# Kernel tuning notes

Hardware: AMD Instinct MI355X
Metric: run time of the kernel (lower is better)

Reference implementation:

```python
import jax, jax.numpy as jnp
import numpy as np

N_NODES = 10000
N_EDGES = 640000
EMB_DIM = 128
NUM_RELS = 500


def setup_inputs() -> dict:
    key = jax.random.key(0)
    k_h, k_s, k_d, k_e, k_f, k_r = jax.random.split(key, 6)
    h = jax.random.normal(k_h, (N_NODES, EMB_DIM), dtype=jnp.float32)
    src = jax.random.randint(k_s, (N_EDGES,), 0, N_NODES, dtype=jnp.int64)
    dst = jax.random.randint(k_d, (N_EDGES,), 0, N_NODES, dtype=jnp.int64)
    etype = jax.random.randint(k_e, (N_EDGES,), 0, NUM_RELS, dtype=jnp.int64)
    fwd_rel = jax.random.normal(k_f, (NUM_RELS, EMB_DIM), dtype=jnp.float32)
    rev_rel = jax.random.normal(k_r, (NUM_RELS, EMB_DIM), dtype=jnp.float32)
    return {"h": h, "src": src, "dst": dst, "etype": etype,
            "fwd_rel": fwd_rel, "rev_rel": rev_rel}


def reference(h, src, dst, etype, fwd_rel, rev_rel):
    # DistMult forward-direction scoring (num_rels > 1 branch):
    #   w  = fwd_rel[etype]                  -> [E, D]
    #   ht = h[src] * w                      (u_mul_e)
    #   score[e] = <ht[e], h[dst[e]]>        (e_dot_v)
    w = fwd_rel[etype]                       # [E, D] gather
    h_u = h[src]                             # [E, D] gather
    h_v = h[dst]                             # [E, D] gather
    score = jnp.einsum("ed,ed,ed->e", h_u, w, h_v)  # [E]
    return score
```

## Files before the change

### kernel.cpp

```cpp
#include <hip/hip_runtime.h>


constexpr int EMB_DIM  = 128;
constexpr int HALF_DIM = 64;

__global__ __launch_bounds__(256) void distmult_half_kernel(
    const float* __restrict__ h,
    const int*   __restrict__ src,
    const int*   __restrict__ dst,
    const int*   __restrict__ etype,
    const float* __restrict__ fwd_rel,
    float*       __restrict__ partial,
    int n_edges)
{
    const int b    = blockIdx.x;
    const int g    = b >> 3;
    const int r    = b & 7;
    const int half = (r >= 4);
    const int idx  = g * 4 + (r & 3);

    const int team = threadIdx.x >> 4;
    const int lane = threadIdx.x & 15;

    const int e0 = idx * 32 + team * 2;
    const int e1 = e0 + 1;
    if (e0 >= n_edges) return;

    const int doff = half * HALF_DIM + lane * 4;

    const int s0 = src[e0];
    const int d0 = dst[e0];
    const int t0 = etype[e0];

    float4 a0, b0, c0;
    a0 = *reinterpret_cast<const float4*>(h       + (size_t)s0 * EMB_DIM + doff);
    b0 = *reinterpret_cast<const float4*>(fwd_rel + (size_t)t0 * EMB_DIM + doff);
    c0 = *reinterpret_cast<const float4*>(h       + (size_t)d0 * EMB_DIM + doff);

    float acc0 = a0.x * b0.x * c0.x + a0.y * b0.y * c0.y
               + a0.z * b0.z * c0.z + a0.w * b0.w * c0.w;

    float acc1 = 0.0f;
    const bool has1 = (e1 < n_edges);
    if (has1) {
        const int s1 = src[e1];
        const int d1 = dst[e1];
        const int t1 = etype[e1];
        float4 a1 = *reinterpret_cast<const float4*>(h       + (size_t)s1 * EMB_DIM + doff);
        float4 b1 = *reinterpret_cast<const float4*>(fwd_rel + (size_t)t1 * EMB_DIM + doff);
        float4 c1 = *reinterpret_cast<const float4*>(h       + (size_t)d1 * EMB_DIM + doff);
        acc1 = a1.x * b1.x * c1.x + a1.y * b1.y * c1.y
             + a1.z * b1.z * c1.z + a1.w * b1.w * c1.w;
    }

    #pragma unroll
    for (int off = 8; off > 0; off >>= 1) {
        acc0 += __shfl_down(acc0, off, 16);
        acc1 += __shfl_down(acc1, off, 16);
    }

    if (lane == 0) {
        float* p = partial + (size_t)half * n_edges;
        p[e0] = acc0;
        if (has1) p[e1] = acc1;
    }
}

__global__ __launch_bounds__(256) void combine_kernel(
    const float* __restrict__ p, float* __restrict__ out, int n_edges)
{
    const int n4 = n_edges >> 2;
    const float4* p0 = reinterpret_cast<const float4*>(p);
    const float4* p1 = reinterpret_cast<const float4*>(p + n_edges);
    float4* o = reinterpret_cast<float4*>(out);
    for (int i = blockIdx.x * blockDim.x + threadIdx.x; i < n4;
         i += gridDim.x * blockDim.x) {
        float4 x = p0[i], y = p1[i];
        o[i] = make_float4(x.x + y.x, x.y + y.y, x.z + y.z, x.w + y.w);
    }
    for (int i = (n4 << 2) + blockIdx.x * blockDim.x + threadIdx.x; i < n_edges;
         i += gridDim.x * blockDim.x) {
        out[i] = p[i] + p[n_edges + i];
    }
}

__global__ __launch_bounds__(256) void distmult_score_kernel(
    const float* __restrict__ h,
    const int*   __restrict__ src,
    const int*   __restrict__ dst,
    const int*   __restrict__ etype,
    const float* __restrict__ fwd_rel,
    float*       __restrict__ out,
    int n_edges)
{
    const int tid  = blockIdx.x * blockDim.x + threadIdx.x;
    const int lane = threadIdx.x & 63;
    const int half = lane >> 5;
    const int sub  = lane & 31;
    const int edge = (tid >> 6) * 2 + half;
    if (edge >= n_edges) return;

    const int s = src[edge];
    const int d = dst[edge];
    const int e = etype[edge];

    const float4 a = reinterpret_cast<const float4*>(h       + (size_t)s * EMB_DIM)[sub];
    const float4 b = reinterpret_cast<const float4*>(fwd_rel + (size_t)e * EMB_DIM)[sub];
    const float4 c = reinterpret_cast<const float4*>(h       + (size_t)d * EMB_DIM)[sub];

    float acc = a.x * b.x * c.x + a.y * b.y * c.y
              + a.z * b.z * c.z + a.w * b.w * c.w;
    #pragma unroll
    for (int off = 16; off > 0; off >>= 1)
        acc += __shfl_down(acc, off, 32);
    if (sub == 0) out[edge] = acc;
}

extern "C" void kernel_launch(void* const* d_in, const int* in_sizes, int n_in,
                              void* d_out, int out_size, void* d_ws, size_t ws_size,
                              hipStream_t stream) {
    const float* h       = (const float*)d_in[0];
    const int*   src     = (const int*)d_in[1];
    const int*   dst     = (const int*)d_in[2];
    const int*   etype   = (const int*)d_in[3];
    const float* fwd_rel = (const float*)d_in[4];
    float* out = (float*)d_out;

    const int n_edges = in_sizes[1];
    const size_t need = (size_t)2 * n_edges * sizeof(float);

    if (ws_size >= need) {
        float* partial = (float*)d_ws;
        const int blocks_per_half = (n_edges + 31) / 32;
        const int groups = (blocks_per_half + 3) / 4;
        const int grid = groups * 8;
        distmult_half_kernel<<<grid, 256, 0, stream>>>(
            h, src, dst, etype, fwd_rel, partial, n_edges);
        const int cgrid = ((n_edges / 4) + 255) / 256;
        combine_kernel<<<cgrid, 256, 0, stream>>>(partial, out, n_edges);
    } else {
        const int grid = (n_edges + 7) / 8;
        distmult_score_kernel<<<grid, 256, 0, stream>>>(
            h, src, dst, etype, fwd_rel, out, n_edges);
    }
}
```

Measured before the change: 111.9 us.

## Stage relation table half in LDS and use a persistent grid with 4 edges per team

The half-dimension scoring kernel becomes persistent: 256 blocks of 1024 threads. Each block first copies its half of the relation embedding table into shared memory (about 128KB), so relation-vector lookups read LDS instead of global memory. Each 16-lane team then loops over groups of 4 edges, loading indices with int4 vector loads, issuing 8 row gathers at once and writing the 4 scores with one float4 store. The risks are the per-block startup cost of filling LDS before any work begins, lower occupancy from one large LDS-heavy block per CU, and a fallback path now needed when the relation count exceeds 500.

```diff
diff --git a/kernel.cpp b/kernel.cpp
--- a/kernel.cpp
+++ b/kernel.cpp
@@ -1,68 +1,101 @@
 #include <hip/hip_runtime.h>
 
 
-constexpr int EMB_DIM  = 128;
-constexpr int HALF_DIM = 64;
+constexpr int EMB_DIM      = 128;
+constexpr int HALF_DIM     = 64;
+constexpr int MAX_RELS     = 500;
+constexpr int BLOCKS_TOTAL = 256;
+constexpr int BLK_THREADS  = 1024;
 
-__global__ __launch_bounds__(256) void distmult_half_kernel(
+__global__ __launch_bounds__(BLK_THREADS) void distmult_lds_kernel(
     const float* __restrict__ h,
     const int*   __restrict__ src,
     const int*   __restrict__ dst,
     const int*   __restrict__ etype,
     const float* __restrict__ fwd_rel,
     float*       __restrict__ partial,
-    int n_edges)
+    int n_edges, int n_rels)
 {
+    __shared__ float w_lds[MAX_RELS * HALF_DIM];
+
     const int b    = blockIdx.x;
     const int g    = b >> 3;
     const int r    = b & 7;
     const int half = (r >= 4);
     const int idx  = g * 4 + (r & 3);
 
+    {
+        const int slots = n_rels * (HALF_DIM / 4);
+        for (int s = threadIdx.x; s < slots; s += BLK_THREADS) {
+            const int row = s >> 4;
+            const int c   = s & 15;
+            float4 v = *reinterpret_cast<const float4*>(
+                fwd_rel + (size_t)row * EMB_DIM + half * HALF_DIM + c * 4);
+            *reinterpret_cast<float4*>(w_lds + row * HALF_DIM + c * 4) = v;
+        }
+    }
+    __syncthreads();
+
     const int team = threadIdx.x >> 4;
     const int lane = threadIdx.x & 15;
 
-    const int e0 = idx * 32 + team * 2;
-    const int e1 = e0 + 1;
-    if (e0 >= n_edges) return;
+    const float* hp = h + half * HALF_DIM + lane * 4;
+    const float* wl = w_lds + lane * 4;
+    float* p = partial + (size_t)half * n_edges;
 
-    const int doff = half * HALF_DIM + lane * 4;
+    const int stride = (BLOCKS_TOTAL / 2) * (BLK_THREADS / 16) * 4;
 
-    const int s0 = src[e0];
-    const int d0 = dst[e0];
-    const int t0 = etype[e0];
+    for (int e0 = idx * (BLK_THREADS / 16) * 4 + team * 4; e0 < n_edges;
+         e0 += stride) {
+        if (e0 + 3 < n_edges) {
+            const int4 s4 = *reinterpret_cast<const int4*>(src   + e0);
+            const int4 d4 = *reinterpret_cast<const int4*>(dst   + e0);
+            const int4 t4 = *reinterpret_cast<const int4*>(etype + e0);
 
-    float4 a0, b0, c0;
-    a0 = *reinterpret_cast<const float4*>(h       + (size_t)s0 * EMB_DIM + doff);
-    b0 = *reinterpret_cast<const float4*>(fwd_rel + (size_t)t0 * EMB_DIM + doff);
-    c0 = *reinterpret_cast<const float4*>(h       + (size_t)d0 * EMB_DIM + doff);
+            float4 a0 = *reinterpret_cast<const float4*>(hp + (size_t)s4.x * EMB_DIM);
+            float4 a1 = *reinterpret_cast<const float4*>(hp + (size_t)s4.y * EMB_DIM);
+            float4 a2 = *reinterpret_cast<const float4*>(hp + (size_t)s4.z * EMB_DIM);
+            float4 a3 = *reinterpret_cast<const float4*>(hp + (size_t)s4.w * EMB_DIM);
+            float4 c0 = *reinterpret_cast<const float4*>(hp + (size_t)d4.x * EMB_DIM);
+            float4 c1 = *reinterpret_cast<const float4*>(hp + (size_t)d4.y * EMB_DIM);
+            float4 c2 = *reinterpret_cast<const float4*>(hp + (size_t)d4.z * EMB_DIM);
+            float4 c3 = *reinterpret_cast<const float4*>(hp + (size_t)d4.w * EMB_DIM);
 
-    float acc0 = a0.x * b0.x * c0.x + a0.y * b0.y * c0.y
-               + a0.z * b0.z * c0.z + a0.w * b0.w * c0.w;
+            float4 b0 = *reinterpret_cast<const float4*>(wl + (size_t)t4.x * HALF_DIM);
+            float4 b1 = *reinterpret_cast<const float4*>(wl + (size_t)t4.y * HALF_DIM);
+            float4 b2 = *reinterpret_cast<const float4*>(wl + (size_t)t4.z * HALF_DIM);
+            float4 b3 = *reinterpret_cast<const float4*>(wl + (size_t)t4.w * HALF_DIM);
 
-    float acc1 = 0.0f;
-    const bool has1 = (e1 < n_edges);
-    if (has1) {
-        const int s1 = src[e1];
-        const int d1 = dst[e1];
-        const int t1 = etype[e1];
-        float4 a1 = *reinterpret_cast<const float4*>(h       + (size_t)s1 * EMB_DIM + doff);
-        float4 b1 = *reinterpret_cast<const float4*>(fwd_rel + (size_t)t1 * EMB_DIM + doff);
-        float4 c1 = *reinterpret_cast<const float4*>(h       + (size_t)d1 * EMB_DIM + doff);
-        acc1 = a1.x * b1.x * c1.x + a1.y * b1.y * c1.y
-             + a1.z * b1.z * c1.z + a1.w * b1.w * c1.w;
-    }
+            float acc0 = a0.x*b0.x*c0.x + a0.y*b0.y*c0.y + a0.z*b0.z*c0.z + a0.w*b0.w*c0.w;
+            float acc1 = a1.x*b1.x*c1.x + a1.y*b1.y*c1.y + a1.z*b1.z*c1.z + a1.w*b1.w*c1.w;
+            float acc2 = a2.x*b2.x*c2.x + a2.y*b2.y*c2.y + a2.z*b2.z*c2.z + a2.w*b2.w*c2.w;
+            float acc3 = a3.x*b3.x*c3.x + a3.y*b3.y*c3.y + a3.z*b3.z*c3.z + a3.w*b3.w*c3.w;
 
-    #pragma unroll
-    for (int off = 8; off > 0; off >>= 1) {
-        acc0 += __shfl_down(acc0, off, 16);
-        acc1 += __shfl_down(acc1, off, 16);
-    }
-
-    if (lane == 0) {
-        float* p = partial + (size_t)half * n_edges;
-        p[e0] = acc0;
-        if (has1) p[e1] = acc1;
+            #pragma unroll
+            for (int off = 8; off > 0; off >>= 1) {
+                acc0 += __shfl_down(acc0, off, 16);
+                acc1 += __shfl_down(acc1, off, 16);
+                acc2 += __shfl_down(acc2, off, 16);
+                acc3 += __shfl_down(acc3, off, 16);
+            }
+            if (lane == 0)
+                *reinterpret_cast<float4*>(p + e0) =
+                    make_float4(acc0, acc1, acc2, acc3);
+        } else {
+            for (int k = 0; k < 4; ++k) {
+                const int e = e0 + k;
+                if (e >= n_edges) break;
+                const int s = src[e], d = dst[e], t = etype[e];
+                float4 a  = *reinterpret_cast<const float4*>(hp + (size_t)s * EMB_DIM);
+                float4 c  = *reinterpret_cast<const float4*>(hp + (size_t)d * EMB_DIM);
+                float4 bb = *reinterpret_cast<const float4*>(wl + (size_t)t * HALF_DIM);
+                float acc = a.x*bb.x*c.x + a.y*bb.y*c.y + a.z*bb.z*c.z + a.w*bb.w*c.w;
+                #pragma unroll
+                for (int off = 8; off > 0; off >>= 1)
+                    acc += __shfl_down(acc, off, 16);
+                if (lane == 0) p[e] = acc;
+            }
+        }
     }
 }
 
@@ -108,8 +141,7 @@
     const float4 b = reinterpret_cast<const float4*>(fwd_rel + (size_t)e * EMB_DIM)[sub];
     const float4 c = reinterpret_cast<const float4*>(h       + (size_t)d * EMB_DIM)[sub];
 
-    float acc = a.x * b.x * c.x + a.y * b.y * c.y
-              + a.z * b.z * c.z + a.w * b.w * c.w;
+    float acc = a.x*b.x*c.x + a.y*b.y*c.y + a.z*b.z*c.z + a.w*b.w*c.w;
     #pragma unroll
     for (int off = 16; off > 0; off >>= 1)
         acc += __shfl_down(acc, off, 32);
@@ -127,15 +159,13 @@
     float* out = (float*)d_out;
 
     const int n_edges = in_sizes[1];
+    const int n_rels  = in_sizes[4] / EMB_DIM;
     const size_t need = (size_t)2 * n_edges * sizeof(float);
 
-    if (ws_size >= need) {
+    if (ws_size >= need && n_rels <= MAX_RELS) {
         float* partial = (float*)d_ws;
-        const int blocks_per_half = (n_edges + 31) / 32;
-        const int groups = (blocks_per_half + 3) / 4;
-        const int grid = groups * 8;
-        distmult_half_kernel<<<grid, 256, 0, stream>>>(
-            h, src, dst, etype, fwd_rel, partial, n_edges);
+        distmult_lds_kernel<<<BLOCKS_TOTAL, BLK_THREADS, 0, stream>>>(
+            h, src, dst, etype, fwd_rel, partial, n_edges, n_rels);
         const int cgrid = ((n_edges / 4) + 255) / 256;
         combine_kernel<<<cgrid, 256, 0, stream>>>(partial, out, n_edges);
     } else {
```

Result: faster. 107.0 us (-4.5%).
